# Performance work log

Hardware: AMD Instinct MI355X
Metric: run time of the kernel (lower is better)

## Reference

```python
import jax, jax.numpy as jnp
import numpy as np

WIN = 8          # window_size
DIM = 96         # embedding dim
HEADS = 3        # num_heads
N = WIN * WIN    # tokens per window
B_ = 8192        # total windows (2 images * 64*64 windows)
NUM_WIN = 4096   # windows per image (mask leading dim)


def _relative_position_index():
    # Same construction as the torch module (meshgrid default 'ij').
    ch = np.arange(WIN)
    coords = np.stack(np.meshgrid(ch, ch, indexing="ij"))          # [2, W, W]
    flat = coords.reshape(2, -1)                                     # [2, N]
    rel = flat[:, :, None] - flat[:, None, :]                        # [2, N, N]
    rel = rel.transpose(1, 2, 0).astype(np.int32)                    # [N, N, 2]
    rel[:, :, 0] += WIN - 1
    rel[:, :, 1] += WIN - 1
    rel[:, :, 0] *= 2 * WIN - 1
    return rel.sum(-1)                                               # [N, N] int32


def setup_inputs() -> dict:
    key = jax.random.key(0)
    ks = jax.random.split(key, 8)
    x = jax.random.normal(ks[0], (B_, N, DIM), dtype=jnp.float32)
    mask = jax.random.normal(ks[1], (NUM_WIN, N, N), dtype=jnp.float32)
    s = 0.02
    qkv_w = jax.random.normal(ks[2], (3 * DIM, DIM), dtype=jnp.float32) * s
    qkv_b = jax.random.normal(ks[3], (3 * DIM,), dtype=jnp.float32) * s
    proj_w = jax.random.normal(ks[4], (DIM, DIM), dtype=jnp.float32) * s
    proj_b = jax.random.normal(ks[5], (DIM,), dtype=jnp.float32) * s
    n_bias = (2 * WIN - 1) * (2 * WIN - 1)  # 225
    bias_table = jax.random.normal(ks[6], (n_bias, HEADS), dtype=jnp.float32) * s
    rel_idx = jnp.asarray(_relative_position_index())  # [N, N] int32
    return {"x": x, "mask": mask, "qkv_w": qkv_w, "qkv_b": qkv_b,
            "proj_w": proj_w, "proj_b": proj_b, "bias_table": bias_table,
            "rel_idx": rel_idx}


def reference(x, mask, qkv_w, qkv_b, proj_w, proj_b, bias_table, rel_idx):
    Bw, n, C = x.shape
    hd = C // HEADS
    scale = hd ** (-0.5)
    qkv = (x @ qkv_w.T + qkv_b).reshape(Bw, n, 3, HEADS, hd)
    qkv = jnp.transpose(qkv, (2, 0, 3, 1, 4))
    q, k, v = qkv[0], qkv[1], qkv[2]
    attn = jnp.einsum("bhqd,bhkd->bhqk", q * scale, k)              # [Bw, H, n, n]
    # relative position bias gather: [n, n, H] -> [H, n, n]
    bias = bias_table[rel_idx.reshape(-1)].reshape(n, n, HEADS)
    attn = attn + jnp.transpose(bias, (2, 0, 1))[None]
    # shift mask: broadcast over (batch, heads)
    nw = mask.shape[0]
    attn = attn.reshape(Bw // nw, nw, HEADS, n, n) + mask[None, :, None]
    attn = attn.reshape(Bw, HEADS, n, n)
    attn = jax.nn.softmax(attn, axis=-1)
    out = jnp.einsum("bhqk,bhkd->bhqd", attn, v)                    # [Bw, H, n, hd]
    out = jnp.transpose(out, (0, 2, 1, 3)).reshape(Bw, n, C)
    return out @ proj_w.T + proj_b
```

## Files before the change

### kernel.cpp

```cpp
#include <hip/hip_runtime.h>

typedef __attribute__((ext_vector_type(8))) short short8v;
typedef __attribute__((ext_vector_type(4))) float f32x4;

#define INVLN2 1.4426950408889634f

__device__ __forceinline__ ushort f2bf(float f) {
  union { float f; unsigned int u; } c; c.f = f;
  return (ushort)((c.u + 0x7FFFu + ((c.u >> 16) & 1u)) >> 16);
}

__device__ __forceinline__ unsigned cvtpk(float a, float b) {
  unsigned r;
  asm("v_cvt_pk_bf16_f32 %0, %1, %2" : "=v"(r) : "v"(a), "v"(b));
  return r;
}

__device__ __forceinline__ float exp2w(float x) {
#if __has_builtin(__builtin_amdgcn_exp2f)
  return __builtin_amdgcn_exp2f(x);
#else
  return __expf(x * 0.6931471805599453f);
#endif
}

__device__ __forceinline__ short8v bits8(unsigned a, unsigned b, unsigned c, unsigned d) {
  union { unsigned u[4]; short8v s; } cv;
  cv.u[0] = a; cv.u[1] = b; cv.u[2] = c; cv.u[3] = d;
  return cv.s;
}

__global__ __launch_bounds__(256) void setup_k(
    const float* __restrict__ qkv_w, const float* __restrict__ proj_w,
    const float* __restrict__ bias_table, const int* __restrict__ rel_idx,
    const float* __restrict__ qkv_b,
    ushort* __restrict__ qkv_wb, ushort* __restrict__ proj_wb,
    float* __restrict__ bias_comb, float* __restrict__ qkv_bs) {
  const float qs = 0.17677669529663687f * INVLN2;
  int idx = blockIdx.x * 256 + threadIdx.x;
  if (idx < 27648) {
    qkv_wb[idx] = f2bf(qkv_w[idx] * (idx < 9216 ? qs : 1.0f));
  } else if (idx < 36864) {
    int i = idx - 27648;
    proj_wb[i] = f2bf(proj_w[i]);
  } else if (idx < 49152) {
    int i = idx - 36864;
    int h = i / 4096, rc = i % 4096;
    bias_comb[i] = bias_table[rel_idx[rc] * 3 + h] * INVLN2;
  } else if (idx < 49440) {
    int i = idx - 49152;
    qkv_bs[i] = qkv_b[i] * (i < 96 ? qs : 1.0f);
  }
}

__global__ __launch_bounds__(256, 3) void winattn(
    const float* __restrict__ x, const float* __restrict__ mask,
    const ushort* __restrict__ qkv_wb, const ushort* __restrict__ proj_wb,
    const float* __restrict__ bias_comb, const float* __restrict__ qkv_bs,
    const float* __restrict__ proj_b, float* __restrict__ out) {
  __shared__ ushort klds[2][64][104];
  __shared__ ushort vts[2][96][64];

  const int bb = blockIdx.x;
  const int t = threadIdx.x;
  const int w = t >> 6;
  const int lane = t & 63;
  const int l15 = lane & 15;
  const int g = lane >> 4;
  const int qrow = w * 16 + l15;

  const bool ghi = (g >= 2);
  const int srcA = l15 + 16 * ((g & 1) * 2);
  const int srcB = srcA + 16;

  short8v xa[2][3];
  #pragma unroll
  for (int u = 0; u < 2; ++u) {
    const float* xr = x + ((size_t)(bb + u * 4096) * 64 + qrow) * 96 + g * 8;
    #pragma unroll
    for (int ks3 = 0; ks3 < 3; ++ks3) {
      float4 a0 = *reinterpret_cast<const float4*>(xr + ks3 * 32);
      float4 a1 = *reinterpret_cast<const float4*>(xr + ks3 * 32 + 4);
      xa[u][ks3] = bits8(cvtpk(a0.x, a0.y), cvtpk(a0.z, a0.w),
                         cvtpk(a1.x, a1.y), cvtpk(a1.z, a1.w));
    }
  }

  unsigned qpk[2][6][2];
  #pragma unroll
  for (int nt = 0; nt < 6; ++nt) {
    short8v bf[3];
    #pragma unroll
    for (int ks3 = 0; ks3 < 3; ++ks3)
      bf[ks3] = *reinterpret_cast<const short8v*>(qkv_wb + (nt * 16 + l15) * 96 + ks3 * 32 + g * 8);
    float4 qb = *reinterpret_cast<const float4*>(qkv_bs + nt * 16 + g * 4);
    #pragma unroll
    for (int u = 0; u < 2; ++u) {
      f32x4 acc = {0.f, 0.f, 0.f, 0.f};
      #pragma unroll
      for (int ks3 = 0; ks3 < 3; ++ks3)
        acc = __builtin_amdgcn_mfma_f32_16x16x32_bf16(bf[ks3], xa[u][ks3], acc, 0, 0, 0);
      qpk[u][nt][0] = cvtpk(acc[0] + qb.x, acc[1] + qb.y);
      qpk[u][nt][1] = cvtpk(acc[2] + qb.z, acc[3] + qb.w);
    }
  }
  short8v qf[2][3];
  #pragma unroll
  for (int u = 0; u < 2; ++u)
    #pragma unroll
    for (int h = 0; h < 3; ++h) {
      unsigned dm[4];
      #pragma unroll
      for (int m = 0; m < 4; ++m) {
        const int sl = (m < 2) ? srcA : srcB;
        unsigned lo = __shfl(qpk[u][2 * h + 0][m & 1], sl);
        unsigned hi = __shfl(qpk[u][2 * h + 1][m & 1], sl);
        dm[m] = ghi ? hi : lo;
      }
      qf[u][h] = bits8(dm[0], dm[1], dm[2], dm[3]);
    }

  #pragma unroll
  for (int nt = 6; nt < 12; ++nt) {
    short8v bf[3];
    #pragma unroll
    for (int ks3 = 0; ks3 < 3; ++ks3)
      bf[ks3] = *reinterpret_cast<const short8v*>(qkv_wb + (nt * 16 + l15) * 96 + ks3 * 32 + g * 8);
    float4 qb = *reinterpret_cast<const float4*>(qkv_bs + nt * 16 + g * 4);
    #pragma unroll
    for (int u = 0; u < 2; ++u) {
      f32x4 acc = {0.f, 0.f, 0.f, 0.f};
      #pragma unroll
      for (int ks3 = 0; ks3 < 3; ++ks3)
        acc = __builtin_amdgcn_mfma_f32_16x16x32_bf16(bf[ks3], xa[u][ks3], acc, 0, 0, 0);
      uint2 pk = make_uint2(cvtpk(acc[0] + qb.x, acc[1] + qb.y),
                            cvtpk(acc[2] + qb.z, acc[3] + qb.w));
      *reinterpret_cast<uint2*>(&klds[u][qrow][(nt - 6) * 16 + g * 4]) = pk;
    }
  }

  #pragma unroll
  for (int nt = 12; nt < 18; ++nt) {
    const int cw = nt * 16 + l15;
    const int vc = cw - 192;
    const int tk = (w * 16 + g * 4) ^ ((vc & 7) << 3);
    short8v bf[3];
    #pragma unroll
    for (int ks3 = 0; ks3 < 3; ++ks3)
      bf[ks3] = *reinterpret_cast<const short8v*>(qkv_wb + cw * 96 + ks3 * 32 + g * 8);
    const float vb = qkv_bs[cw];
    #pragma unroll
    for (int u = 0; u < 2; ++u) {
      f32x4 acc = {0.f, 0.f, 0.f, 0.f};
      #pragma unroll
      for (int ks3 = 0; ks3 < 3; ++ks3)
        acc = __builtin_amdgcn_mfma_f32_16x16x32_bf16(xa[u][ks3], bf[ks3], acc, 0, 0, 0);
      uint2 pk = make_uint2(cvtpk(acc[0] + vb, acc[1] + vb),
                            cvtpk(acc[2] + vb, acc[3] + vb));
      *reinterpret_cast<uint2*>(&vts[u][vc][tk]) = pk;
    }
  }

  const float* mrow = mask + (size_t)bb * 4096 + qrow * 64;
  float mk[4][4];
  #pragma unroll
  for (int tj = 0; tj < 4; ++tj) {
    float4 m4 = *reinterpret_cast<const float4*>(mrow + tj * 16 + g * 4);
    mk[tj][0] = m4.x * INVLN2; mk[tj][1] = m4.y * INVLN2;
    mk[tj][2] = m4.z * INVLN2; mk[tj][3] = m4.w * INVLN2;
  }

  __syncthreads();

  const float* bcb0 = bias_comb + qrow * 64;
  short8v ofv[3][2];

  #pragma unroll
  for (int h = 0; h < 3; ++h) {
    f32x4 s[2][4];
    #pragma unroll
    for (int tj = 0; tj < 4; ++tj) {
      #pragma unroll
      for (int u = 0; u < 2; ++u) {
        short8v kf = *reinterpret_cast<const short8v*>(&klds[u][tj * 16 + l15][h * 32 + g * 8]);
        f32x4 z = {0.f, 0.f, 0.f, 0.f};
        s[u][tj] = __builtin_amdgcn_mfma_f32_16x16x32_bf16(kf, qf[u][h], z, 0, 0, 0);
      }
    }
    #pragma unroll
    for (int tj = 0; tj < 4; ++tj) {
      float4 bc4 = *reinterpret_cast<const float4*>(bcb0 + h * 4096 + tj * 16 + g * 4);
      float bm[4] = {bc4.x + mk[tj][0], bc4.y + mk[tj][1],
                     bc4.z + mk[tj][2], bc4.w + mk[tj][3]};
      #pragma unroll
      for (int u = 0; u < 2; ++u)
        #pragma unroll
        for (int r = 0; r < 4; ++r) s[u][tj][r] += bm[r];
    }
    float inv[2];
    #pragma unroll
    for (int u = 0; u < 2; ++u) {
      #pragma unroll
      for (int tj = 0; tj < 4; ++tj)
        #pragma unroll
        for (int r = 0; r < 4; ++r) s[u][tj][r] = exp2w(s[u][tj][r]);
      float sm = ((s[u][0][0] + s[u][0][1]) + (s[u][0][2] + s[u][0][3]))
               + ((s[u][1][0] + s[u][1][1]) + (s[u][1][2] + s[u][1][3]))
               + ((s[u][2][0] + s[u][2][1]) + (s[u][2][2] + s[u][2][3]))
               + ((s[u][3][0] + s[u][3][1]) + (s[u][3][2] + s[u][3][3]));
      sm += __shfl_xor(sm, 16);
      sm += __shfl_xor(sm, 32);
      inv[u] = __builtin_amdgcn_rcpf(sm);
    }
    unsigned ppk[2][4][2];
    #pragma unroll
    for (int u = 0; u < 2; ++u)
      #pragma unroll
      for (int tj = 0; tj < 4; ++tj) {
        ppk[u][tj][0] = cvtpk(s[u][tj][0], s[u][tj][1]);
        ppk[u][tj][1] = cvtpk(s[u][tj][2], s[u][tj][3]);
      }
    short8v pfv[2][2];
    #pragma unroll
    for (int u = 0; u < 2; ++u)
      #pragma unroll
      for (int ks2 = 0; ks2 < 2; ++ks2) {
        unsigned dm[4];
        #pragma unroll
        for (int m = 0; m < 4; ++m) {
          const int sl = (m < 2) ? srcA : srcB;
          unsigned lo = __shfl(ppk[u][ks2 * 2 + 0][m & 1], sl);
          unsigned hi = __shfl(ppk[u][ks2 * 2 + 1][m & 1], sl);
          dm[m] = ghi ? hi : lo;
        }
        pfv[u][ks2] = bits8(dm[0], dm[1], dm[2], dm[3]);
      }
    f32x4 oacc[2][2];
    #pragma unroll
    for (int u = 0; u < 2; ++u)
      #pragma unroll
      for (int nt = 0; nt < 2; ++nt) {
        const int vc = h * 32 + nt * 16 + l15;
        f32x4 o = {0.f, 0.f, 0.f, 0.f};
        #pragma unroll
        for (int ks2 = 0; ks2 < 2; ++ks2) {
          const int tk = (ks2 * 32 + g * 8) ^ ((vc & 7) << 3);
          short8v vf = *reinterpret_cast<const short8v*>(&vts[u][vc][tk]);
          o = __builtin_amdgcn_mfma_f32_16x16x32_bf16(vf, pfv[u][ks2], o, 0, 0, 0);
        }
        oacc[u][nt] = o;
      }
    #pragma unroll
    for (int u = 0; u < 2; ++u) {
      unsigned opk[2][2];
      #pragma unroll
      for (int nt = 0; nt < 2; ++nt) {
        opk[nt][0] = cvtpk(oacc[u][nt][0] * inv[u], oacc[u][nt][1] * inv[u]);
        opk[nt][1] = cvtpk(oacc[u][nt][2] * inv[u], oacc[u][nt][3] * inv[u]);
      }
      unsigned dm[4];
      #pragma unroll
      for (int m = 0; m < 4; ++m) {
        const int sl = (m < 2) ? srcA : srcB;
        unsigned lo = __shfl(opk[0][m & 1], sl);
        unsigned hi = __shfl(opk[1][m & 1], sl);
        dm[m] = ghi ? hi : lo;
      }
      ofv[h][u] = bits8(dm[0], dm[1], dm[2], dm[3]);
    }
  }

  f32x4 pacc[2][6];
  #pragma unroll
  for (int u = 0; u < 2; ++u)
    #pragma unroll
    for (int nt2 = 0; nt2 < 6; ++nt2) pacc[u][nt2] = (f32x4){0.f, 0.f, 0.f, 0.f};
  #pragma unroll
  for (int h = 0; h < 3; ++h) {
    #pragma unroll
    for (int nt2 = 0; nt2 < 6; ++nt2) {
      short8v pfw = *reinterpret_cast<const short8v*>(proj_wb + (nt2 * 16 + l15) * 96 + h * 32 + g * 8);
      #pragma unroll
      for (int u = 0; u < 2; ++u)
        pacc[u][nt2] = __builtin_amdgcn_mfma_f32_16x16x32_bf16(ofv[h][u], pfw, pacc[u][nt2], 0, 0, 0);
    }
  }

  float pb[6];
  #pragma unroll
  for (int nt2 = 0; nt2 < 6; ++nt2) pb[nt2] = proj_b[nt2 * 16 + l15];
  #pragma unroll
  for (int u = 0; u < 2; ++u) {
    float* ob = out + (size_t)(bb + u * 4096) * 6144 + (w * 16 + g * 4) * 96 + l15;
    #pragma unroll
    for (int nt2 = 0; nt2 < 6; ++nt2)
      #pragma unroll
      for (int r = 0; r < 4; ++r)
        ob[r * 96 + nt2 * 16] = pacc[u][nt2][r] + pb[nt2];
  }
}

extern "C" void kernel_launch(void* const* d_in, const int* in_sizes, int n_in,
                              void* d_out, int out_size, void* d_ws, size_t ws_size,
                              hipStream_t stream) {
  const float* x          = (const float*)d_in[0];
  const float* mask       = (const float*)d_in[1];
  const float* qkv_w      = (const float*)d_in[2];
  const float* qkv_b      = (const float*)d_in[3];
  const float* proj_w     = (const float*)d_in[4];
  const float* proj_b     = (const float*)d_in[5];
  const float* bias_table = (const float*)d_in[6];
  const int*   rel_idx    = (const int*)d_in[7];

  char* ws = (char*)d_ws;
  ushort* qkv_wb    = (ushort*)ws;
  ushort* proj_wb   = (ushort*)(ws + 55296);
  float*  bias_comb = (float*)(ws + 55296 + 18432);
  float*  qkv_bs    = (float*)(ws + 55296 + 18432 + 49152);

  setup_k<<<194, 256, 0, stream>>>(qkv_w, proj_w, bias_table, rel_idx, qkv_b,
                                   qkv_wb, proj_wb, bias_comb, qkv_bs);
  winattn<<<4096, 256, 0, stream>>>(x, mask, qkv_wb, proj_wb,
                                    bias_comb, qkv_bs, proj_b, (float*)d_out);
}
```

Baseline: 180.2 us.

## Prefetch weights, mask and bias early; relax occupancy to free registers

The mask row is now loaded together with x at kernel start, so it is in flight during the QKV projection. The three projection loops are merged into one loop over 18 tiles that double-buffers the next weight and bias fragment in registers. All relative-bias values are loaded and combined with the mask before the barrier. Launch bounds drop from 3 to 2 waves-per-SIMD minimum to make room for the extra live registers, which trades occupancy for memory-latency hiding.

After: 167.5 us. 7.0% less time.

```diff
diff --git a/kernel.cpp b/kernel.cpp
--- a/kernel.cpp
+++ b/kernel.cpp
@@ -53,7 +53,7 @@
   }
 }
 
-__global__ __launch_bounds__(256, 3) void winattn(
+__global__ __launch_bounds__(256, 2) void winattn(
     const float* __restrict__ x, const float* __restrict__ mask,
     const ushort* __restrict__ qkv_wb, const ushort* __restrict__ proj_wb,
     const float* __restrict__ bias_comb, const float* __restrict__ qkv_bs,
@@ -73,37 +73,95 @@
   const int srcA = l15 + 16 * ((g & 1) * 2);
   const int srcB = srcA + 16;
 
-  short8v xa[2][3];
+  float4 xr4[2][3][2];
   #pragma unroll
   for (int u = 0; u < 2; ++u) {
     const float* xr = x + ((size_t)(bb + u * 4096) * 64 + qrow) * 96 + g * 8;
     #pragma unroll
     for (int ks3 = 0; ks3 < 3; ++ks3) {
-      float4 a0 = *reinterpret_cast<const float4*>(xr + ks3 * 32);
-      float4 a1 = *reinterpret_cast<const float4*>(xr + ks3 * 32 + 4);
+      xr4[u][ks3][0] = *reinterpret_cast<const float4*>(xr + ks3 * 32);
+      xr4[u][ks3][1] = *reinterpret_cast<const float4*>(xr + ks3 * 32 + 4);
+    }
+  }
+  const float* mrow = mask + (size_t)bb * 4096 + qrow * 64;
+  float4 mk4[4];
+  #pragma unroll
+  for (int tj = 0; tj < 4; ++tj)
+    mk4[tj] = *reinterpret_cast<const float4*>(mrow + tj * 16 + g * 4);
+
+  short8v xa[2][3];
+  #pragma unroll
+  for (int u = 0; u < 2; ++u)
+    #pragma unroll
+    for (int ks3 = 0; ks3 < 3; ++ks3) {
+      const float4 a0 = xr4[u][ks3][0], a1 = xr4[u][ks3][1];
       xa[u][ks3] = bits8(cvtpk(a0.x, a0.y), cvtpk(a0.z, a0.w),
                          cvtpk(a1.x, a1.y), cvtpk(a1.z, a1.w));
     }
-  }
 
   unsigned qpk[2][6][2];
-  #pragma unroll
-  for (int nt = 0; nt < 6; ++nt) {
-    short8v bf[3];
-    #pragma unroll
-    for (int ks3 = 0; ks3 < 3; ++ks3)
-      bf[ks3] = *reinterpret_cast<const short8v*>(qkv_wb + (nt * 16 + l15) * 96 + ks3 * 32 + g * 8);
-    float4 qb = *reinterpret_cast<const float4*>(qkv_bs + nt * 16 + g * 4);
-    #pragma unroll
-    for (int u = 0; u < 2; ++u) {
-      f32x4 acc = {0.f, 0.f, 0.f, 0.f};
-      #pragma unroll
-      for (int ks3 = 0; ks3 < 3; ++ks3)
-        acc = __builtin_amdgcn_mfma_f32_16x16x32_bf16(bf[ks3], xa[u][ks3], acc, 0, 0, 0);
-      qpk[u][nt][0] = cvtpk(acc[0] + qb.x, acc[1] + qb.y);
-      qpk[u][nt][1] = cvtpk(acc[2] + qb.z, acc[3] + qb.w);
-    }
-  }
+  short8v bfA[3];
+  float4 qbA = {0.f, 0.f, 0.f, 0.f}, qbB;
+  float vbA = 0.f, vbB;
+  {
+    const ushort* wr = qkv_wb + l15 * 96 + g * 8;
+    bfA[0] = *reinterpret_cast<const short8v*>(wr);
+    bfA[1] = *reinterpret_cast<const short8v*>(wr + 32);
+    bfA[2] = *reinterpret_cast<const short8v*>(wr + 64);
+    qbA = *reinterpret_cast<const float4*>(qkv_bs + g * 4);
+  }
+  #pragma unroll
+  for (int nt = 0; nt < 18; ++nt) {
+    short8v bfB[3];
+    if (nt < 17) {
+      const ushort* wr = qkv_wb + ((nt + 1) * 16 + l15) * 96 + g * 8;
+      bfB[0] = *reinterpret_cast<const short8v*>(wr);
+      bfB[1] = *reinterpret_cast<const short8v*>(wr + 32);
+      bfB[2] = *reinterpret_cast<const short8v*>(wr + 64);
+      if (nt + 1 < 12) qbB = *reinterpret_cast<const float4*>(qkv_bs + (nt + 1) * 16 + g * 4);
+      else             vbB = qkv_bs[(nt + 1) * 16 + l15];
+    }
+    if (nt < 6) {
+      #pragma unroll
+      for (int u = 0; u < 2; ++u) {
+        f32x4 acc = {0.f, 0.f, 0.f, 0.f};
+        #pragma unroll
+        for (int ks3 = 0; ks3 < 3; ++ks3)
+          acc = __builtin_amdgcn_mfma_f32_16x16x32_bf16(bfA[ks3], xa[u][ks3], acc, 0, 0, 0);
+        qpk[u][nt][0] = cvtpk(acc[0] + qbA.x, acc[1] + qbA.y);
+        qpk[u][nt][1] = cvtpk(acc[2] + qbA.z, acc[3] + qbA.w);
+      }
+    } else if (nt < 12) {
+      #pragma unroll
+      for (int u = 0; u < 2; ++u) {
+        f32x4 acc = {0.f, 0.f, 0.f, 0.f};
+        #pragma unroll
+        for (int ks3 = 0; ks3 < 3; ++ks3)
+          acc = __builtin_amdgcn_mfma_f32_16x16x32_bf16(bfA[ks3], xa[u][ks3], acc, 0, 0, 0);
+        uint2 pk = make_uint2(cvtpk(acc[0] + qbA.x, acc[1] + qbA.y),
+                              cvtpk(acc[2] + qbA.z, acc[3] + qbA.w));
+        *reinterpret_cast<uint2*>(&klds[u][qrow][(nt - 6) * 16 + g * 4]) = pk;
+      }
+    } else {
+      const int vc = nt * 16 + l15 - 192;
+      const int tk = (w * 16 + g * 4) ^ ((vc & 7) << 3);
+      #pragma unroll
+      for (int u = 0; u < 2; ++u) {
+        f32x4 acc = {0.f, 0.f, 0.f, 0.f};
+        #pragma unroll
+        for (int ks3 = 0; ks3 < 3; ++ks3)
+          acc = __builtin_amdgcn_mfma_f32_16x16x32_bf16(xa[u][ks3], bfA[ks3], acc, 0, 0, 0);
+        uint2 pk = make_uint2(cvtpk(acc[0] + vbA, acc[1] + vbA),
+                              cvtpk(acc[2] + vbA, acc[3] + vbA));
+        *reinterpret_cast<uint2*>(&vts[u][vc][tk]) = pk;
+      }
+    }
+    if (nt < 17) {
+      bfA[0] = bfB[0]; bfA[1] = bfB[1]; bfA[2] = bfB[2];
+      qbA = qbB; vbA = vbB;
+    }
+  }
+
   short8v qf[2][3];
   #pragma unroll
   for (int u = 0; u < 2; ++u)
@@ -120,59 +178,26 @@
       qf[u][h] = bits8(dm[0], dm[1], dm[2], dm[3]);
     }
 
-  #pragma unroll
-  for (int nt = 6; nt < 12; ++nt) {
-    short8v bf[3];
-    #pragma unroll
-    for (int ks3 = 0; ks3 < 3; ++ks3)
-      bf[ks3] = *reinterpret_cast<const short8v*>(qkv_wb + (nt * 16 + l15) * 96 + ks3 * 32 + g * 8);
-    float4 qb = *reinterpret_cast<const float4*>(qkv_bs + nt * 16 + g * 4);
-    #pragma unroll
-    for (int u = 0; u < 2; ++u) {
-      f32x4 acc = {0.f, 0.f, 0.f, 0.f};
-      #pragma unroll
-      for (int ks3 = 0; ks3 < 3; ++ks3)
-        acc = __builtin_amdgcn_mfma_f32_16x16x32_bf16(bf[ks3], xa[u][ks3], acc, 0, 0, 0);
-      uint2 pk = make_uint2(cvtpk(acc[0] + qb.x, acc[1] + qb.y),
-                            cvtpk(acc[2] + qb.z, acc[3] + qb.w));
-      *reinterpret_cast<uint2*>(&klds[u][qrow][(nt - 6) * 16 + g * 4]) = pk;
-    }
-  }
-
-  #pragma unroll
-  for (int nt = 12; nt < 18; ++nt) {
-    const int cw = nt * 16 + l15;
-    const int vc = cw - 192;
-    const int tk = (w * 16 + g * 4) ^ ((vc & 7) << 3);
-    short8v bf[3];
-    #pragma unroll
-    for (int ks3 = 0; ks3 < 3; ++ks3)
-      bf[ks3] = *reinterpret_cast<const short8v*>(qkv_wb + cw * 96 + ks3 * 32 + g * 8);
-    const float vb = qkv_bs[cw];
-    #pragma unroll
-    for (int u = 0; u < 2; ++u) {
-      f32x4 acc = {0.f, 0.f, 0.f, 0.f};
-      #pragma unroll
-      for (int ks3 = 0; ks3 < 3; ++ks3)
-        acc = __builtin_amdgcn_mfma_f32_16x16x32_bf16(xa[u][ks3], bf[ks3], acc, 0, 0, 0);
-      uint2 pk = make_uint2(cvtpk(acc[0] + vb, acc[1] + vb),
-                            cvtpk(acc[2] + vb, acc[3] + vb));
-      *reinterpret_cast<uint2*>(&vts[u][vc][tk]) = pk;
-    }
-  }
-
-  const float* mrow = mask + (size_t)bb * 4096 + qrow * 64;
-  float mk[4][4];
-  #pragma unroll
-  for (int tj = 0; tj < 4; ++tj) {
-    float4 m4 = *reinterpret_cast<const float4*>(mrow + tj * 16 + g * 4);
-    mk[tj][0] = m4.x * INVLN2; mk[tj][1] = m4.y * INVLN2;
-    mk[tj][2] = m4.z * INVLN2; mk[tj][3] = m4.w * INVLN2;
-  }
+  const float* bcb0 = bias_comb + qrow * 64;
+  float4 bc4[3][4];
+  #pragma unroll
+  for (int h = 0; h < 3; ++h)
+    #pragma unroll
+    for (int tj = 0; tj < 4; ++tj)
+      bc4[h][tj] = *reinterpret_cast<const float4*>(bcb0 + h * 4096 + tj * 16 + g * 4);
+  float bmk[3][4][4];
+  #pragma unroll
+  for (int h = 0; h < 3; ++h)
+    #pragma unroll
+    for (int tj = 0; tj < 4; ++tj) {
+      bmk[h][tj][0] = bc4[h][tj].x + mk4[tj].x * INVLN2;
+      bmk[h][tj][1] = bc4[h][tj].y + mk4[tj].y * INVLN2;
+      bmk[h][tj][2] = bc4[h][tj].z + mk4[tj].z * INVLN2;
+      bmk[h][tj][3] = bc4[h][tj].w + mk4[tj].w * INVLN2;
+    }
 
   __syncthreads();
 
-  const float* bcb0 = bias_comb + qrow * 64;
   short8v ofv[3][2];
 
   #pragma unroll
@@ -188,15 +213,11 @@
       }
     }
     #pragma unroll
-    for (int tj = 0; tj < 4; ++tj) {
-      float4 bc4 = *reinterpret_cast<const float4*>(bcb0 + h * 4096 + tj * 16 + g * 4);
-      float bm[4] = {bc4.x + mk[tj][0], bc4.y + mk[tj][1],
-                     bc4.z + mk[tj][2], bc4.w + mk[tj][3]};
+    for (int tj = 0; tj < 4; ++tj)
       #pragma unroll
       for (int u = 0; u < 2; ++u)
         #pragma unroll
-        for (int r = 0; r < 4; ++r) s[u][tj][r] += bm[r];
-    }
+        for (int r = 0; r < 4; ++r) s[u][tj][r] += bmk[h][tj][r];
     float inv[2];
     #pragma unroll
     for (int u = 0; u < 2; ++u) {
```
